# Performance work log

Measured on AMD Instinct MI355X. Metric: run time of the kernel, lower is better.

The kernel has to match this reference:

```python
import jax, jax.numpy as jnp
import numpy as np

N_NODES = 50000
N_EDGES = 800000
N_GRAPHS = 512
F_IN = 16
E_DIM = 64
D = 128          # encoder_dim
L_DIM = 64       # latent_dim
MP_STEPS = 3
S2S_STEPS = 3
NEG_SLOPE = 0.01


def _leaky(v):
    return jax.nn.leaky_relu(v, NEG_SLOPE)


def setup_inputs() -> dict:
    key = jax.random.key(0)
    ks = jax.random.split(key, 24)

    def w(k, fan_in, shape):
        return jax.random.normal(k, shape, jnp.float32) / np.sqrt(fan_in)

    inp = {
        "x": jax.random.normal(ks[0], (N_NODES, F_IN), jnp.float32),
        "edge_index": jax.random.randint(ks[1], (2, N_EDGES), 0, N_NODES, jnp.int64),
        "edge_attr": jax.random.normal(ks[2], (N_EDGES, 4), jnp.float32),
        "batch": jnp.sort(jax.random.randint(ks[3], (N_NODES,), 0, N_GRAPHS, jnp.int64)),
        # embedding: Linear(F_IN -> E_DIM); weights stored [in, out]
        "W_emb": w(ks[4], F_IN, (F_IN, E_DIM)),
        "b_emb": jnp.zeros((E_DIM,), jnp.float32),
        # first: Linear(E_DIM -> D)
        "W_first": w(ks[5], E_DIM, (E_DIM, D)),
        "b_first": jnp.zeros((D,), jnp.float32),
        # SAGEConv: lin_l (aggregated neighbors, with bias), lin_r (root, no bias)
        "W_l": w(ks[6], D, (D, D)),
        "b_l": jnp.zeros((D,), jnp.float32),
        "W_r": w(ks[7], D, (D, D)),
        # GRU (1 layer): gates ordered r,z,n as in torch
        "gru_Wih": w(ks[8], D, (D, 3 * D)),
        "gru_Whh": w(ks[9], D, (D, 3 * D)),
        "gru_bih": jnp.zeros((3 * D,), jnp.float32),
        "gru_bhh": jnp.zeros((3 * D,), jnp.float32),
        # Set2Set LSTM: input 2D -> hidden D; gates ordered i,f,g,o as in torch
        "lstm_Wih": w(ks[10], 2 * D, (2 * D, 4 * D)),
        "lstm_Whh": w(ks[11], D, (D, 4 * D)),
        "lstm_bih": jnp.zeros((4 * D,), jnp.float32),
        "lstm_bhh": jnp.zeros((4 * D,), jnp.float32),
        # linear: Linear(2D -> D), final: Linear(D -> L_DIM)
        "W_lin": w(ks[12], 2 * D, (2 * D, D)),
        "b_lin": jnp.zeros((D,), jnp.float32),
        "W_fin": w(ks[13], D, (D, L_DIM)),
        "b_fin": jnp.zeros((L_DIM,), jnp.float32),
    }
    return inp


def _gru_step(x, h, Wih, Whh, bih, bhh):
    gi = x @ Wih + bih
    gh = h @ Whh + bhh
    ir, iz, inn = jnp.split(gi, 3, axis=-1)
    hr, hz, hn = jnp.split(gh, 3, axis=-1)
    r = jax.nn.sigmoid(ir + hr)
    z = jax.nn.sigmoid(iz + hz)
    n = jnp.tanh(inn + r * hn)
    return (1.0 - z) * n + z * h


def _lstm_step(x, h, c, Wih, Whh, bih, bhh):
    g = x @ Wih + bih + h @ Whh + bhh
    i, f, gg, o = jnp.split(g, 4, axis=-1)
    c_new = jax.nn.sigmoid(f) * c + jax.nn.sigmoid(i) * jnp.tanh(gg)
    h_new = jax.nn.sigmoid(o) * jnp.tanh(c_new)
    return h_new, c_new


def reference(x, edge_index, edge_attr, batch,
              W_emb, b_emb, W_first, b_first,
              W_l, b_l, W_r,
              gru_Wih, gru_Whh, gru_bih, gru_bhh,
              lstm_Wih, lstm_Whh, lstm_bih, lstm_bhh,
              W_lin, b_lin, W_fin, b_fin):
    # edge_attr is ignored (PyG SAGEConv does not use it).
    out = _leaky(x @ W_emb + b_emb)        # [N, E_DIM]
    out = _leaky(out @ W_first + b_first)  # [N, D]
    h = out                                # GRU hidden state [N, D]
    src, dst = edge_index[0], edge_index[1]
    for _ in range(MP_STEPS):
        agg = jax.ops.segment_sum(out[src], dst, num_segments=N_NODES)  # [N, D]
        m = jax.nn.relu(agg @ W_l + b_l + out @ W_r)  # SAGEConv(aggr='add') + root
        out = _gru_step(m, h, gru_Wih, gru_Whh, gru_bih, gru_bhh)
        h = out
    # Set2Set pooling over graphs
    q_star = jnp.zeros((N_GRAPHS, 2 * D), out.dtype)
    hh = jnp.zeros((N_GRAPHS, D), out.dtype)
    cc = jnp.zeros((N_GRAPHS, D), out.dtype)
    for _ in range(S2S_STEPS):
        hh, cc = _lstm_step(q_star, hh, cc, lstm_Wih, lstm_Whh, lstm_bih, lstm_bhh)
        e = jnp.sum(out * hh[batch], axis=-1)                             # [N]
        e_max = jax.ops.segment_max(e, batch, num_segments=N_GRAPHS)      # [B]
        a = jnp.exp(e - e_max[batch])
        s = jax.ops.segment_sum(a, batch, num_segments=N_GRAPHS)
        a = a / (s[batch] + 1e-16)                                        # segment softmax
        r = jax.ops.segment_sum(a[:, None] * out, batch, num_segments=N_GRAPHS)  # [B, D]
        q_star = jnp.concatenate([hh, r], axis=-1)                        # [B, 2D]
    out = _leaky(q_star @ W_lin + b_lin)
    return out @ W_fin + b_fin  # [B, L_DIM]
```

## Files before the change

kernel.cpp:

```cpp
#include <hip/hip_runtime.h>
#include <hip/hip_bf16.h>
#include <math.h>

#define N_NODES 50000
#define N_EDGES 800000
#define N_GRAPHS 512
#define F_IN 16
#define E_DIM 64
#define D 128
#define L_DIM 64
#define NEG_SLOPE 0.01f

#define SCAN_N (N_NODES + 1)
#define NBUCK ((N_NODES + 127) >> 7)
#define EPT 4
#define BFT 1024
#define EPB (BFT * EPT)

typedef __hip_bfloat16 bf16;
typedef unsigned int uint;
typedef unsigned short ushort;
typedef __attribute__((ext_vector_type(8))) short short8;
typedef __attribute__((ext_vector_type(4))) float float4v;

__device__ __forceinline__ float b2f(bf16 v) { return __bfloat162float(v); }
__device__ __forceinline__ bf16  f2b(float v) { return __float2bfloat16(v); }
__device__ __forceinline__ short f2bs(float f) { bf16 b = __float2bfloat16(f); return *reinterpret_cast<short*>(&b); }
__device__ __forceinline__ float bs2f(short s) { return __uint_as_float(((uint)(ushort)s) << 16); }
__device__ __forceinline__ float leaky(float v) { return v > 0.f ? v : NEG_SLOPE * v; }

__device__ __forceinline__ float frcp(float x) { return __builtin_amdgcn_rcpf(x); }
__device__ __forceinline__ float sigm(float v) { return frcp(1.f + __expf(-v)); }
__device__ __forceinline__ float ftanh(float v)
{
    v = fminf(15.f, fmaxf(-15.f, v));
    float a = __expf(2.f * v);
    return (a - 1.f) * frcp(a + 1.f);
}

__global__ __launch_bounds__(256) void k_signal(float* outp, int n)
{
    int i = blockIdx.x * 256 + threadIdx.x;
    if (i < n) outp[i] = 1.0f;
}

#define NPE 16
__global__ __launch_bounds__(128) void k_embed(
    const float* __restrict__ x, const float* __restrict__ Wemb, const float* __restrict__ bemb,
    const float* __restrict__ Wfirst, const float* __restrict__ bfirst, bf16* __restrict__ out)
{
    __shared__ float xs[NPE][F_IN];
    __shared__ float ys[NPE][E_DIM];
    int t = threadIdx.x;
    int base = blockIdx.x * NPE;

    for (int i = t; i < NPE * F_IN; i += 128)
        xs[i / F_IN][i % F_IN] = x[(size_t)base * F_IN + i];
    __syncthreads();

    if (t < E_DIM) {
        float acc[NPE];
#pragma unroll
        for (int nn = 0; nn < NPE; nn++) acc[nn] = 0.f;
        for (int k = 0; k < F_IN; k++) {
            float w = Wemb[k * E_DIM + t];
#pragma unroll
            for (int nn = 0; nn < NPE; nn++) acc[nn] += xs[nn][k] * w;
        }
        float bb = bemb[t];
#pragma unroll
        for (int nn = 0; nn < NPE; nn++) ys[nn][t] = leaky(acc[nn] + bb);
    }
    __syncthreads();

    {
        float acc[NPE];
#pragma unroll
        for (int nn = 0; nn < NPE; nn++) acc[nn] = 0.f;
        for (int k = 0; k < E_DIM; k++) {
            float w = Wfirst[k * D + t];
#pragma unroll
            for (int nn = 0; nn < NPE; nn++) acc[nn] += ys[nn][k] * w;
        }
        float bb = bfirst[t];
#pragma unroll
        for (int nn = 0; nn < NPE; nn++)
            out[(size_t)(base + nn) * D + t] = f2b(leaky(acc[nn] + bb));
    }
}

__global__ __launch_bounds__(256) void k_bcount(const int* __restrict__ ei, int* __restrict__ bcnt)
{
    __shared__ int lc[NBUCK];
    for (int i = threadIdx.x; i < NBUCK; i += 256) lc[i] = 0;
    __syncthreads();
    int stride = gridDim.x * 256;
    for (int e = blockIdx.x * 256 + threadIdx.x; e < N_EDGES; e += stride) {
        int d = ei[N_EDGES + e];
        d = d < 0 ? 0 : (d >= N_NODES ? N_NODES - 1 : d);
        atomicAdd(&lc[d >> 7], 1);
    }
    __syncthreads();
    for (int i = threadIdx.x; i < NBUCK; i += 256)
        if (lc[i]) atomicAdd(&bcnt[i + 1], lc[i]);
}

__global__ void k_bscan(int* __restrict__ bcnt)
{
    if (threadIdx.x == 0 && blockIdx.x == 0) {
        int run = 0;
        for (int i = 0; i <= NBUCK; i++) { run += bcnt[i]; bcnt[i] = run; }
    }
}

__global__ __launch_bounds__(BFT) void k_bfill2(
    const int* __restrict__ ei, const int* __restrict__ bstart,
    int* __restrict__ bcur, uint* __restrict__ ebuf)
{
    __shared__ int lcnt[NBUCK];
    __shared__ int lbase[NBUCK];
    int t = threadIdx.x;
    int e0 = blockIdx.x * EPB;

    for (int i = t; i < NBUCK; i += BFT) lcnt[i] = 0;
    __syncthreads();

    uint pk[EPT];
    int bb[EPT];
#pragma unroll
    for (int q = 0; q < EPT; q++) {
        int e = e0 + q * BFT + t;
        bb[q] = -1;
        if (e < N_EDGES) {
            int s = ei[e];
            int d = ei[N_EDGES + e];
            s = s < 0 ? 0 : (s >= N_NODES ? N_NODES - 1 : s);
            d = d < 0 ? 0 : (d >= N_NODES ? N_NODES - 1 : d);
            bb[q] = d >> 7;
            pk[q] = ((uint)(d & 127) << 16) | (uint)s;
            atomicAdd(&lcnt[bb[q]], 1);
        }
    }
    __syncthreads();

    for (int i = t; i < NBUCK; i += BFT) {
        int cv = lcnt[i];
        lbase[i] = cv > 0 ? atomicAdd(&bcur[i], cv) : 0;
    }
    __syncthreads();
    for (int i = t; i < NBUCK; i += BFT) lcnt[i] = 0;
    __syncthreads();

#pragma unroll
    for (int q = 0; q < EPT; q++) {
        if (bb[q] >= 0) {
            int pos = lbase[bb[q]] + atomicAdd(&lcnt[bb[q]], 1);
            int slot = bstart[bb[q]] + pos;
            if (slot >= 0 && slot < N_EDGES) ebuf[slot] = pk[q];
        }
    }
}

__global__ __launch_bounds__(256) void k_csr(
    const int* __restrict__ bstart, const uint* __restrict__ ebuf,
    int* __restrict__ offs, int* __restrict__ srcs)
{
    __shared__ int cnt[128];
    __shared__ int loffs[129];
    int b = blockIdx.x, t = threadIdx.x;
    int e0 = bstart[b], e1 = bstart[b + 1];
    if (t < 128) cnt[t] = 0;
    __syncthreads();
    for (int j = e0 + t; j < e1; j += 256)
        atomicAdd(&cnt[(ebuf[j] >> 16) & 127], 1);
    __syncthreads();
    if (t == 0) {
        int run = 0;
        for (int i = 0; i < 128; i++) { loffs[i] = run; run += cnt[i]; }
        loffs[128] = run;
    }
    __syncthreads();
    int n0 = b << 7;
    if (t < 128) {
        int n = n0 + t;
        if (n <= N_NODES) offs[n] = e0 + loffs[t];
        cnt[t] = 0;
    }
    __syncthreads();
    for (int j = e0 + t; j < e1; j += 256) {
        uint pk = ebuf[j];
        int dl = (pk >> 16) & 127;
        int rank = atomicAdd(&cnt[dl], 1);
        int slot = e0 + loffs[dl] + rank;
        if (slot >= 0 && slot < N_EDGES) srcs[slot] = (int)(pk & 0xffffu);
    }
}

__global__ __launch_bounds__(256) void k_gstart(const int* __restrict__ batch, int* __restrict__ gstart)
{
    int g = blockIdx.x * 256 + threadIdx.x;
    if (g > N_GRAPHS) return;
    int lo = 0, hi = N_NODES;
    while (lo < hi) {
        int mid = (lo + hi) >> 1;
        if (batch[mid] < g) lo = mid + 1; else hi = mid;
    }
    gstart[g] = lo;
}

__global__ __launch_bounds__(256) void k_pack_all(
    const float* __restrict__ Wl, const float* __restrict__ Wr,
    const float* __restrict__ gWih, const float* __restrict__ gWhh,
    short* __restrict__ W1p, short* __restrict__ Wihp, short* __restrict__ Whhp)
{
    int tid = blockIdx.x * 256 + threadIdx.x;
    if (tid < 32768) {
        int j = tid & 7, l = (tid >> 3) & 63, frag = tid >> 9;
        int nb = frag >> 3, kb = frag & 7;
        int k = kb * 32 + ((l >> 4) * 8) + j;
        int n = nb * 16 + (l & 15);
        float v = (k < 128) ? Wl[k * D + n] : Wr[(k - 128) * D + n];
        W1p[tid] = f2bs(v);
    } else {
        int id = tid - 32768;
        const float* W = gWih;
        short* Wp = Wihp;
        if (id >= 49152) { id -= 49152; W = gWhh; Wp = Whhp; }
        int j = id & 7, l = (id >> 3) & 63, f = id >> 9;
        int ph = f >> 2, k0 = f & 3;
        int ct = ph / 3, p = ph - ct * 3;
        int k = k0 * 32 + ((l >> 4) * 8) + j;
        int n = p * 128 + ct * 16 + (l & 15);
        Wp[id] = f2bs(W[k * 384 + n]);
    }
}

__global__ __launch_bounds__(256) void k_gather(
    const bf16* __restrict__ hin, bf16* __restrict__ hagg,
    const int* __restrict__ offs, const int* __restrict__ srcs)
{
    int w = threadIdx.x >> 6, l = threadIdx.x & 63;
    int n = blockIdx.x * 4 + w;
    const ushort* hinu = (const ushort*)hin;
    int j0 = offs[n], j1 = offs[n + 1];
    j0 = j0 < 0 ? 0 : (j0 > N_EDGES ? N_EDGES : j0);
    j1 = j1 < j0 ? j0 : (j1 > N_EDGES ? N_EDGES : j1);

    float lo[8], hi8[8];
#pragma unroll
    for (int i = 0; i < 8; i++) { lo[i] = 0.f; hi8[i] = 0.f; }

    int j = j0;
    for (; j + 7 < j1; j += 8) {
        int ss[8];
        uint vv[8];
#pragma unroll
        for (int i = 0; i < 8; i++) {
            int s = srcs[j + i];
            ss[i] = s < 0 ? 0 : (s >= N_NODES ? N_NODES - 1 : s);
        }
#pragma unroll
        for (int i = 0; i < 8; i++)
            vv[i] = *(const uint*)(hinu + (size_t)ss[i] * D + l * 2);
#pragma unroll
        for (int i = 0; i < 8; i++) {
            lo[i] += __uint_as_float(vv[i] << 16);
            hi8[i] += __uint_as_float(vv[i] & 0xffff0000u);
        }
    }
    for (; j < j1; j++) {
        int s = srcs[j];
        s = s < 0 ? 0 : (s >= N_NODES ? N_NODES - 1 : s);
        uint v = *(const uint*)(hinu + (size_t)s * D + l * 2);
        lo[0] += __uint_as_float(v << 16);
        hi8[0] += __uint_as_float(v & 0xffff0000u);
    }
    float a0 = ((lo[0] + lo[1]) + (lo[2] + lo[3])) + ((lo[4] + lo[5]) + (lo[6] + lo[7]));
    float a1 = ((hi8[0] + hi8[1]) + (hi8[2] + hi8[3])) + ((hi8[4] + hi8[5]) + (hi8[6] + hi8[7]));
    uint ap = ((uint)(ushort)f2bs(a1) << 16) | (ushort)f2bs(a0);
    *(uint*)((ushort*)hagg + (size_t)n * D + l * 2) = ap;
}

#define M_STR 136
__global__ __launch_bounds__(256) void k_sage_gru_mfma(
    const bf16* __restrict__ hin, bf16* __restrict__ hagg_out,
    const short* __restrict__ W1p, const short* __restrict__ Wihp, const short* __restrict__ Whhp,
    const float* __restrict__ bl, const float* __restrict__ bih, const float* __restrict__ bhh)
{
    __shared__ short Msh[64 * M_STR];
    __shared__ short Hsh[64 * M_STR];
    int t = threadIdx.x;
    int w = t >> 6, l = t & 63;
    int rg = w >> 1, cg = w & 1;
    int base = blockIdx.x * 64;
    const ushort* hinu = (const ushort*)hin;
    const ushort* haggu = (const ushort*)hagg_out;
    ushort* houtu = (ushort*)hagg_out;

    int rA = base + rg * 32 + (l & 15);
    int rB = rA + 16;
    int rcA = rA < N_NODES ? rA : N_NODES - 1;
    int rcB = rB < N_NODES ? rB : N_NODES - 1;
    int koff = (l >> 4) * 8;

    short8 afrA[8], afrB[8];
#pragma unroll
    for (int k0 = 0; k0 < 4; k0++) {
        afrA[k0]     = *(const short8*)(haggu + (size_t)rcA * D + k0 * 32 + koff);
        afrB[k0]     = *(const short8*)(haggu + (size_t)rcB * D + k0 * 32 + koff);
        afrA[4 + k0] = *(const short8*)(hinu + (size_t)rcA * D + k0 * 32 + koff);
        afrB[4 + k0] = *(const short8*)(hinu + (size_t)rcB * D + k0 * 32 + koff);
    }

    int mrowA = rg * 32 + (l & 15);
    int mrowB = mrowA + 16;
    int crowA = rg * 32 + (l >> 4) * 4;
    int crowB = crowA + 16;

    if (cg == 0) {
#pragma unroll
        for (int k0 = 0; k0 < 4; k0++) {
            *(short8*)&Hsh[mrowA * M_STR + k0 * 32 + koff] = afrA[4 + k0];
            *(short8*)&Hsh[mrowB * M_STR + k0 * 32 + koff] = afrB[4 + k0];
        }
    }

    const short* w1 = W1p + cg * 16384;
    short8 bA[8], bB[8];
#pragma unroll
    for (int k0 = 0; k0 < 8; k0++)
        bA[k0] = *(const short8*)&w1[k0 * 512 + l * 8];
#pragma unroll
    for (int cti = 0; cti < 4; cti++) {
        int ct = cg * 4 + cti;
        const short8* bc = (cti & 1) ? bB : bA;
        short8* bn = (cti & 1) ? bA : bB;
        if (cti < 3) {
#pragma unroll
            for (int k0 = 0; k0 < 8; k0++)
                bn[k0] = *(const short8*)&w1[(cti + 1) * 4096 + k0 * 512 + l * 8];
        }
        float4v accA = {0.f, 0.f, 0.f, 0.f};
        float4v accB = {0.f, 0.f, 0.f, 0.f};
#pragma unroll
        for (int k0 = 0; k0 < 8; k0++) {
            accA = __builtin_amdgcn_mfma_f32_16x16x32_bf16(afrA[k0], bc[k0], accA, 0, 0, 0);
            accB = __builtin_amdgcn_mfma_f32_16x16x32_bf16(afrB[k0], bc[k0], accB, 0, 0, 0);
        }
        float bb = bl[ct * 16 + (l & 15)];
#pragma unroll
        for (int i = 0; i < 4; i++) {
            float vA = accA[i] + bb;
            float vB = accB[i] + bb;
            Msh[(crowA + i) * M_STR + ct * 16 + (l & 15)] = f2bs(vA > 0.f ? vA : 0.f);
            Msh[(crowB + i) * M_STR + ct * 16 + (l & 15)] = f2bs(vB > 0.f ? vB : 0.f);
        }
    }
    __syncthreads();

    short8 amrA[4], amrB[4];
#pragma unroll
    for (int k0 = 0; k0 < 4; k0++) {
        amrA[k0] = *(const short8*)&Msh[mrowA * M_STR + k0 * 32 + koff];
        amrB[k0] = *(const short8*)&Msh[mrowB * M_STR + k0 * 32 + koff];
    }

    const short* wip = Wihp + cg * 24576;
    const short* whp = Whhp + cg * 24576;
    short8 iA[4], hA[4], iB[4], hB[4];
#pragma unroll
    for (int k0 = 0; k0 < 4; k0++) {
        iA[k0] = *(const short8*)&wip[k0 * 512 + l * 8];
        hA[k0] = *(const short8*)&whp[k0 * 512 + l * 8];
    }
#pragma unroll
    for (int cti = 0; cti < 4; cti++) {
        int ct = cg * 4 + cti;
        int c = ct * 16 + (l & 15);
        float rvA[4], zvA[4], rvB[4], zvB[4];
#pragma unroll
        for (int p = 0; p < 3; p++) {
            int phl = cti * 3 + p;
            const short8* wi = (phl & 1) ? iB : iA;
            const short8* wh = (phl & 1) ? hB : hA;
            short8* win = (phl & 1) ? iA : iB;
            short8* whn = (phl & 1) ? hA : hB;
            if (phl < 11) {
#pragma unroll
                for (int k0 = 0; k0 < 4; k0++) {
                    win[k0] = *(const short8*)&wip[(phl + 1) * 2048 + k0 * 512 + l * 8];
                    whn[k0] = *(const short8*)&whp[(phl + 1) * 2048 + k0 * 512 + l * 8];
                }
            }
            float4v aiA = {0.f, 0.f, 0.f, 0.f};
            float4v ahA = {0.f, 0.f, 0.f, 0.f};
            float4v aiB = {0.f, 0.f, 0.f, 0.f};
            float4v ahB = {0.f, 0.f, 0.f, 0.f};
#pragma unroll
            for (int k0 = 0; k0 < 4; k0++) {
                aiA = __builtin_amdgcn_mfma_f32_16x16x32_bf16(amrA[k0], wi[k0], aiA, 0, 0, 0);
                ahA = __builtin_amdgcn_mfma_f32_16x16x32_bf16(afrA[4 + k0], wh[k0], ahA, 0, 0, 0);
                aiB = __builtin_amdgcn_mfma_f32_16x16x32_bf16(amrB[k0], wi[k0], aiB, 0, 0, 0);
                ahB = __builtin_amdgcn_mfma_f32_16x16x32_bf16(afrB[4 + k0], wh[k0], ahB, 0, 0, 0);
            }
            float bis = bih[p * 128 + c];
            float bhs = bhh[p * 128 + c];
            if (p == 0) {
#pragma unroll
                for (int i = 0; i < 4; i++) {
                    rvA[i] = sigm(aiA[i] + bis + ahA[i] + bhs);
                    rvB[i] = sigm(aiB[i] + bis + ahB[i] + bhs);
                }
            } else if (p == 1) {
#pragma unroll
                for (int i = 0; i < 4; i++) {
                    zvA[i] = sigm(aiA[i] + bis + ahA[i] + bhs);
                    zvB[i] = sigm(aiB[i] + bis + ahB[i] + bhs);
                }
            } else {
#pragma unroll
                for (int i = 0; i < 4; i++) {
                    int gA = base + crowA + i;
                    float h0A = bs2f(Hsh[(crowA + i) * M_STR + c]);
                    float nA = ftanh(aiA[i] + bis + rvA[i] * (ahA[i] + bhs));
                    if (gA < N_NODES)
                        houtu[(size_t)gA * D + c] = (ushort)f2bs((1.f - zvA[i]) * nA + zvA[i] * h0A);
                    int gB = base + crowB + i;
                    float h0B = bs2f(Hsh[(crowB + i) * M_STR + c]);
                    float nB = ftanh(aiB[i] + bis + rvB[i] * (ahB[i] + bhs));
                    if (gB < N_NODES)
                        houtu[(size_t)gB * D + c] = (ushort)f2bs((1.f - zvB[i]) * nB + zvB[i] * h0B);
                }
            }
        }
    }
}

#define POOL_CAP 1024
#define LG2 2
__global__ __launch_bounds__(1024) void k_s2s(
    const float* __restrict__ Wih, const float* __restrict__ Whh,
    const float* __restrict__ bih, const float* __restrict__ bhh,
    const bf16* __restrict__ h, const int* __restrict__ gstart,
    float* __restrict__ qstar, float* __restrict__ hh, float* __restrict__ cc, int first)
{
    int g0 = blockIdx.x * LG2;
    int t = threadIdx.x;
    __shared__ float qs[LG2][2 * D];
    __shared__ float hs[LG2][D];
    __shared__ float part[2][LG2][512];
    __shared__ float hnew[LG2][D];
    __shared__ float e_lds[POOL_CAP];
    __shared__ float redM[16], redS[16];
    __shared__ float rpart[8][D];

    for (int i = t; i < LG2 * 2 * D; i += 1024) {
        int g = i / (2 * D), c = i % (2 * D);
        qs[g][c] = first ? 0.f : qstar[(size_t)(g0 + g) * 2 * D + c];
    }
    for (int i = t; i < LG2 * D; i += 1024) {
        int g = i / D, c = i % D;
        hs[g][c] = first ? 0.f : hh[(size_t)(g0 + g) * D + c];
    }
    __syncthreads();

    int c = t & 511, half = t >> 9;
    float a0 = half ? 0.f : (bih[c] + bhh[c]);
    float a1 = a0;
    int qb = half * 128;
#pragma unroll 4
    for (int i = 0; i < 128; i++) {
        int k = qb + i;
        float wv = Wih[(size_t)k * 512 + c];
        a0 += qs[0][k] * wv;
        a1 += qs[1][k] * wv;
    }
    int hb = half * 64;
#pragma unroll 4
    for (int i = 0; i < 64; i++) {
        int k = hb + i;
        float wv = Whh[(size_t)k * 512 + c];
        a0 += hs[0][k] * wv;
        a1 += hs[1][k] * wv;
    }
    part[half][0][c] = a0;
    part[half][1][c] = a1;
    __syncthreads();

    if (t < LG2 * D) {
        int g = t >> 7, tt = t & 127;
        float gi = part[0][g][tt] + part[1][g][tt];
        float gf = part[0][g][D + tt] + part[1][g][D + tt];
        float gg2 = part[0][g][2 * D + tt] + part[1][g][2 * D + tt];
        float go = part[0][g][3 * D + tt] + part[1][g][3 * D + tt];
        float c_old = first ? 0.f : cc[(size_t)(g0 + g) * D + tt];
        float cn = sigm(gf) * c_old + sigm(gi) * ftanh(gg2);
        float hn = sigm(go) * ftanh(cn);
        cc[(size_t)(g0 + g) * D + tt] = cn;
        hh[(size_t)(g0 + g) * D + tt] = hn;
        qstar[(size_t)(g0 + g) * 2 * D + tt] = hn;
        hnew[g][tt] = hn;
    }
    __syncthreads();

    int w = t >> 6, l = t & 63;
    int dim = t & 127, h8 = t >> 7;
    const ushort* hu = (const ushort*)h;

    for (int gg = 0; gg < LG2; gg++) {
        int g = g0 + gg;
        int s0 = gstart[g], s1 = gstart[g + 1];
        s0 = s0 < 0 ? 0 : (s0 > N_NODES ? N_NODES : s0);
        s1 = s1 < s0 ? s0 : (s1 > N_NODES ? N_NODES : s1);
        int cnt = s1 - s0;

        float hq0 = hnew[gg][l];
        float hq1 = hnew[gg][64 + l];
        float m_run = -INFINITY, s_run = 0.f, racc = 0.f;

        for (int c0 = 0; c0 < cnt; c0 += POOL_CAP) {
            int clen = cnt - c0; if (clen > POOL_CAP) clen = POOL_CAP;

            for (int i = w; i < clen; i += 16) {
                int n = s0 + c0 + i;
                float v = bs2f((short)hu[(size_t)n * D + l]) * hq0
                        + bs2f((short)hu[(size_t)n * D + 64 + l]) * hq1;
#pragma unroll
                for (int off = 32; off > 0; off >>= 1) v += __shfl_down(v, off);
                if (l == 0) e_lds[i] = v;
            }
            __syncthreads();

            float m = -INFINITY;
            for (int i = t; i < clen; i += 1024) m = fmaxf(m, e_lds[i]);
#pragma unroll
            for (int off = 32; off > 0; off >>= 1) m = fmaxf(m, __shfl_down(m, off));
            if (l == 0) redM[w] = m;
            __syncthreads();
            m = -INFINITY;
#pragma unroll
            for (int i = 0; i < 16; i++) m = fmaxf(m, redM[i]);
            float m_new = fmaxf(m_run, m);
            float scale = (m_run == -INFINITY) ? 0.f : __expf(m_run - m_new);
            s_run *= scale;
            racc *= scale;
            __syncthreads();

            float s = 0.f;
            for (int i = t; i < clen; i += 1024) {
                float wv = __expf(e_lds[i] - m_new);
                e_lds[i] = wv;
                s += wv;
            }
#pragma unroll
            for (int off = 32; off > 0; off >>= 1) s += __shfl_down(s, off);
            if (l == 0) redS[w] = s;
            __syncthreads();
#pragma unroll
            for (int i = 0; i < 16; i++) s_run += redS[i];

            for (int i = h8; i < clen; i += 8)
                racc += e_lds[i] * bs2f((short)hu[(size_t)(s0 + c0 + i) * D + dim]);
            m_run = m_new;
            __syncthreads();
        }

        rpart[h8][dim] = racc;
        __syncthreads();
        if (t < D) {
            float inv = 1.f / (s_run + 1e-16f);
            float r = 0.f;
#pragma unroll
            for (int i = 0; i < 8; i++) r += rpart[i][t];
            qstar[(size_t)g * 2 * D + D + t] = r * inv;
        }
        __syncthreads();
    }
}

__global__ __launch_bounds__(128) void k_final(
    const float* __restrict__ qstar, const float* __restrict__ Wlin, const float* __restrict__ blin,
    const float* __restrict__ Wfin, const float* __restrict__ bfin, float* __restrict__ outp)
{
    int g = blockIdx.x, t = threadIdx.x;
    __shared__ float qs[2 * D], ts[D];
    qs[t] = qstar[(size_t)g * 2 * D + t];
    qs[D + t] = qstar[(size_t)g * 2 * D + D + t];
    __syncthreads();

    float acc = blin[t];
    for (int k = 0; k < 2 * D; k++) acc += qs[k] * Wlin[(size_t)k * D + t];
    ts[t] = leaky(acc);
    __syncthreads();

    if (t < L_DIM) {
        float a2 = bfin[t];
        for (int k = 0; k < D; k++) a2 += ts[k] * Wfin[(size_t)k * L_DIM + t];
        outp[(size_t)g * L_DIM + t] = a2;
    }
}

extern "C" void kernel_launch(void* const* d_in, const int* in_sizes, int n_in,
                              void* d_out, int out_size, void* d_ws, size_t ws_size,
                              hipStream_t stream)
{
    const float* x      = (const float*)d_in[0];
    const int*   ei     = (const int*)d_in[1];
    const int*   batch  = (const int*)d_in[3];
    const float* Wemb   = (const float*)d_in[4];
    const float* bemb   = (const float*)d_in[5];
    const float* Wfirst = (const float*)d_in[6];
    const float* bfirst = (const float*)d_in[7];
    const float* Wl     = (const float*)d_in[8];
    const float* bl     = (const float*)d_in[9];
    const float* Wr     = (const float*)d_in[10];
    const float* gWih   = (const float*)d_in[11];
    const float* gWhh   = (const float*)d_in[12];
    const float* gbih   = (const float*)d_in[13];
    const float* gbhh   = (const float*)d_in[14];
    const float* lWih   = (const float*)d_in[15];
    const float* lWhh   = (const float*)d_in[16];
    const float* lbih   = (const float*)d_in[17];
    const float* lbhh   = (const float*)d_in[18];
    const float* Wlin   = (const float*)d_in[19];
    const float* blin   = (const float*)d_in[20];
    const float* Wfin   = (const float*)d_in[21];
    const float* bfin   = (const float*)d_in[22];
    float* outp = (float*)d_out;

    size_t o = 0;
    char* base = (char*)d_ws;
    auto carve = [&](size_t bytes) { void* p = base + o; o += (bytes + 255) & ~(size_t)255; return p; };
    bf16*  h0     = (bf16*)carve((size_t)N_NODES * D * sizeof(bf16));
    bf16*  h1     = (bf16*)carve((size_t)N_NODES * D * sizeof(bf16));
    int*   offs   = (int*)carve((size_t)SCAN_N * sizeof(int));
    int*   srcs   = (int*)carve((size_t)N_EDGES * sizeof(int));
    int*   bcnt   = (int*)carve((size_t)(NBUCK + 1) * sizeof(int));
    int*   bcur   = (int*)carve((size_t)NBUCK * sizeof(int));
    uint*  ebuf   = (uint*)carve((size_t)N_EDGES * sizeof(uint));
    float* hh     = (float*)carve((size_t)N_GRAPHS * D * sizeof(float));
    float* cc     = (float*)carve((size_t)N_GRAPHS * D * sizeof(float));
    float* qstar  = (float*)carve((size_t)N_GRAPHS * 2 * D * sizeof(float));
    int*   gstart = (int*)carve((size_t)(N_GRAPHS + 1) * sizeof(int));
    short* W1p    = (short*)carve((size_t)256 * 128 * sizeof(short));
    short* Wihp   = (short*)carve((size_t)128 * 384 * sizeof(short));
    short* Whhp   = (short*)carve((size_t)128 * 384 * sizeof(short));
    size_t need = o;

    if (ws_size < need) {
        k_signal<<<(out_size + 255) / 256, 256, 0, stream>>>(outp, out_size);
        return;
    }

    k_embed<<<N_NODES / NPE, 128, 0, stream>>>(x, Wemb, bemb, Wfirst, bfirst, h0);

    k_pack_all<<<(32768 + 98304) / 256, 256, 0, stream>>>(Wl, Wr, gWih, gWhh, W1p, Wihp, Whhp);

    hipMemsetAsync(bcnt, 0, (size_t)((char*)ebuf - (char*)bcnt), stream);
    k_bcount<<<128, 256, 0, stream>>>(ei, bcnt);
    k_bscan<<<1, 64, 0, stream>>>(bcnt);
    k_bfill2<<<(N_EDGES + EPB - 1) / EPB, BFT, 0, stream>>>(ei, bcnt, bcur, ebuf);
    k_csr<<<NBUCK, 256, 0, stream>>>(bcnt, ebuf, offs, srcs);

    k_gstart<<<(N_GRAPHS + 1 + 255) / 256, 256, 0, stream>>>(batch, gstart);

    bf16* hc = h0; bf16* hn = h1;
    for (int s = 0; s < 3; s++) {
        k_gather<<<N_NODES / 4, 256, 0, stream>>>(hc, hn, offs, srcs);
        k_sage_gru_mfma<<<(N_NODES + 63) / 64, 256, 0, stream>>>(
            hc, hn, W1p, Wihp, Whhp, bl, gbih, gbhh);
        bf16* tmp = hc; hc = hn; hn = tmp;
    }

    for (int s = 0; s < 3; s++) {
        k_s2s<<<N_GRAPHS / LG2, 1024, 0, stream>>>(lWih, lWhh, lbih, lbhh,
                                                   hc, gstart, qstar, hh, cc, s == 0);
    }

    k_final<<<N_GRAPHS, 128, 0, stream>>>(qstar, Wlin, blin, Wfin, bfin, outp);
}
```

Before: 497.8 us.

## Split fused SAGE+GRU kernel into two kernels with LDS-staged weights

The fused SAGE+GRU MFMA kernel becomes two kernels. The SAGE linear layer writes its ReLU output to a new global buffer, and a separate GRU kernel launched over 4 column quarters per row tile reads it back. Both kernels stage their packed weight slices in LDS instead of streaming them from global memory into registers per wave. The goal is more parallelism and less register pressure for the GRU phase. The cost is an extra global write and read of the N×D message tensor, an extra launch per step, and the node features being reloaded by each of the four GRU blocks.

```diff
diff --git a/kernel.cpp b/kernel.cpp
--- a/kernel.cpp
+++ b/kernel.cpp
@@ -281,156 +281,172 @@
     *(uint*)((ushort*)hagg + (size_t)n * D + l * 2) = ap;
 }
 
-#define M_STR 136
-__global__ __launch_bounds__(256) void k_sage_gru_mfma(
-    const bf16* __restrict__ hin, bf16* __restrict__ hagg_out,
-    const short* __restrict__ W1p, const short* __restrict__ Wihp, const short* __restrict__ Whhp,
-    const float* __restrict__ bl, const float* __restrict__ bih, const float* __restrict__ bhh)
-{
-    __shared__ short Msh[64 * M_STR];
-    __shared__ short Hsh[64 * M_STR];
+__global__ __launch_bounds__(256) void k_sage1(
+    const bf16* __restrict__ hagg, const bf16* __restrict__ hin,
+    const short* __restrict__ W1p, const float* __restrict__ bl,
+    bf16* __restrict__ mout)
+{
+    __shared__ short8 w1s[4096];
     int t = threadIdx.x;
+    const short8* w1g = (const short8*)W1p;
+#pragma unroll
+    for (int i = 0; i < 16; i++)
+        w1s[i * 256 + t] = w1g[i * 256 + t];
+
     int w = t >> 6, l = t & 63;
     int rg = w >> 1, cg = w & 1;
     int base = blockIdx.x * 64;
-    const ushort* hinu = (const ushort*)hin;
-    const ushort* haggu = (const ushort*)hagg_out;
-    ushort* houtu = (ushort*)hagg_out;
-
     int rA = base + rg * 32 + (l & 15);
     int rB = rA + 16;
     int rcA = rA < N_NODES ? rA : N_NODES - 1;
     int rcB = rB < N_NODES ? rB : N_NODES - 1;
     int koff = (l >> 4) * 8;
+    const ushort* aggu = (const ushort*)hagg;
+    const ushort* hu = (const ushort*)hin;
+    ushort* mo = (ushort*)mout;
 
     short8 afrA[8], afrB[8];
 #pragma unroll
     for (int k0 = 0; k0 < 4; k0++) {
-        afrA[k0]     = *(const short8*)(haggu + (size_t)rcA * D + k0 * 32 + koff);
-        afrB[k0]     = *(const short8*)(haggu + (size_t)rcB * D + k0 * 32 + koff);
-        afrA[4 + k0] = *(const short8*)(hinu + (size_t)rcA * D + k0 * 32 + koff);
-        afrB[4 + k0] = *(const short8*)(hinu + (size_t)rcB * D + k0 * 32 + koff);
-    }
-
-    int mrowA = rg * 32 + (l & 15);
-    int mrowB = mrowA + 16;
+        afrA[k0]     = *(const short8*)(aggu + (size_t)rcA * D + k0 * 32 + koff);
+        afrB[k0]     = *(const short8*)(aggu + (size_t)rcB * D + k0 * 32 + koff);
+        afrA[4 + k0] = *(const short8*)(hu + (size_t)rcA * D + k0 * 32 + koff);
+        afrB[4 + k0] = *(const short8*)(hu + (size_t)rcB * D + k0 * 32 + koff);
+    }
+    __syncthreads();
+
+    const short* w1 = (const short*)w1s;
     int crowA = rg * 32 + (l >> 4) * 4;
     int crowB = crowA + 16;
-
-    if (cg == 0) {
-#pragma unroll
-        for (int k0 = 0; k0 < 4; k0++) {
-            *(short8*)&Hsh[mrowA * M_STR + k0 * 32 + koff] = afrA[4 + k0];
-            *(short8*)&Hsh[mrowB * M_STR + k0 * 32 + koff] = afrB[4 + k0];
-        }
-    }
-
-    const short* w1 = W1p + cg * 16384;
-    short8 bA[8], bB[8];
-#pragma unroll
-    for (int k0 = 0; k0 < 8; k0++)
-        bA[k0] = *(const short8*)&w1[k0 * 512 + l * 8];
 #pragma unroll
     for (int cti = 0; cti < 4; cti++) {
         int ct = cg * 4 + cti;
-        const short8* bc = (cti & 1) ? bB : bA;
-        short8* bn = (cti & 1) ? bA : bB;
-        if (cti < 3) {
-#pragma unroll
-            for (int k0 = 0; k0 < 8; k0++)
-                bn[k0] = *(const short8*)&w1[(cti + 1) * 4096 + k0 * 512 + l * 8];
-        }
+        short8 bw[8];
+#pragma unroll
+        for (int k0 = 0; k0 < 8; k0++)
+            bw[k0] = *(const short8*)&w1[(ct * 8 + k0) * 512 + l * 8];
         float4v accA = {0.f, 0.f, 0.f, 0.f};
         float4v accB = {0.f, 0.f, 0.f, 0.f};
 #pragma unroll
         for (int k0 = 0; k0 < 8; k0++) {
-            accA = __builtin_amdgcn_mfma_f32_16x16x32_bf16(afrA[k0], bc[k0], accA, 0, 0, 0);
-            accB = __builtin_amdgcn_mfma_f32_16x16x32_bf16(afrB[k0], bc[k0], accB, 0, 0, 0);
+            accA = __builtin_amdgcn_mfma_f32_16x16x32_bf16(afrA[k0], bw[k0], accA, 0, 0, 0);
+            accB = __builtin_amdgcn_mfma_f32_16x16x32_bf16(afrB[k0], bw[k0], accB, 0, 0, 0);
         }
         float bb = bl[ct * 16 + (l & 15)];
 #pragma unroll
         for (int i = 0; i < 4; i++) {
             float vA = accA[i] + bb;
             float vB = accB[i] + bb;
-            Msh[(crowA + i) * M_STR + ct * 16 + (l & 15)] = f2bs(vA > 0.f ? vA : 0.f);
-            Msh[(crowB + i) * M_STR + ct * 16 + (l & 15)] = f2bs(vB > 0.f ? vB : 0.f);
-        }
-    }
-    __syncthreads();
-
-    short8 amrA[4], amrB[4];
+            int gA = base + crowA + i;
+            int gB = base + crowB + i;
+            if (gA < N_NODES) mo[(size_t)gA * D + ct * 16 + (l & 15)] = (ushort)f2bs(vA > 0.f ? vA : 0.f);
+            if (gB < N_NODES) mo[(size_t)gB * D + ct * 16 + (l & 15)] = (ushort)f2bs(vB > 0.f ? vB : 0.f);
+        }
+    }
+}
+
+__global__ __launch_bounds__(256) void k_gru2(
+    const bf16* __restrict__ m, const bf16* __restrict__ hin,
+    const short* __restrict__ Wihp, const short* __restrict__ Whhp,
+    const float* __restrict__ bih, const float* __restrict__ bhh,
+    bf16* __restrict__ hout)
+{
+    __shared__ short8 wis[1536];
+    __shared__ short8 whs[1536];
+    int t = threadIdx.x;
+    int tile = blockIdx.x >> 2, cq = blockIdx.x & 3;
+    const short8* wig = (const short8*)(Wihp + cq * 12288);
+    const short8* whg = (const short8*)(Whhp + cq * 12288);
+#pragma unroll
+    for (int i = 0; i < 6; i++) {
+        wis[i * 256 + t] = wig[i * 256 + t];
+        whs[i * 256 + t] = whg[i * 256 + t];
+    }
+
+    int w = t >> 6, l = t & 63;
+    int rg = w >> 1, cs = w & 1;
+    int base = tile * 64;
+    int rA = base + rg * 32 + (l & 15);
+    int rB = rA + 16;
+    int rcA = rA < N_NODES ? rA : N_NODES - 1;
+    int rcB = rB < N_NODES ? rB : N_NODES - 1;
+    int koff = (l >> 4) * 8;
+    int ct = cq * 2 + cs;
+    int c = ct * 16 + (l & 15);
+
+    const ushort* mu = (const ushort*)m;
+    const ushort* hu = (const ushort*)hin;
+    ushort* ho = (ushort*)hout;
+
+    short8 amrA[4], amrB[4], ahfA[4], ahfB[4];
 #pragma unroll
     for (int k0 = 0; k0 < 4; k0++) {
-        amrA[k0] = *(const short8*)&Msh[mrowA * M_STR + k0 * 32 + koff];
-        amrB[k0] = *(const short8*)&Msh[mrowB * M_STR + k0 * 32 + koff];
-    }
-
-    const short* wip = Wihp + cg * 24576;
-    const short* whp = Whhp + cg * 24576;
-    short8 iA[4], hA[4], iB[4], hB[4];
-#pragma unroll
-    for (int k0 = 0; k0 < 4; k0++) {
-        iA[k0] = *(const short8*)&wip[k0 * 512 + l * 8];
-        hA[k0] = *(const short8*)&whp[k0 * 512 + l * 8];
-    }
-#pragma unroll
-    for (int cti = 0; cti < 4; cti++) {
-        int ct = cg * 4 + cti;
-        int c = ct * 16 + (l & 15);
-        float rvA[4], zvA[4], rvB[4], zvB[4];
-#pragma unroll
-        for (int p = 0; p < 3; p++) {
-            int phl = cti * 3 + p;
-            const short8* wi = (phl & 1) ? iB : iA;
-            const short8* wh = (phl & 1) ? hB : hA;
-            short8* win = (phl & 1) ? iA : iB;
-            short8* whn = (phl & 1) ? hA : hB;
-            if (phl < 11) {
-#pragma unroll
-                for (int k0 = 0; k0 < 4; k0++) {
-                    win[k0] = *(const short8*)&wip[(phl + 1) * 2048 + k0 * 512 + l * 8];
-                    whn[k0] = *(const short8*)&whp[(phl + 1) * 2048 + k0 * 512 + l * 8];
-                }
+        amrA[k0] = *(const short8*)(mu + (size_t)rcA * D + k0 * 32 + koff);
+        amrB[k0] = *(const short8*)(mu + (size_t)rcB * D + k0 * 32 + koff);
+        ahfA[k0] = *(const short8*)(hu + (size_t)rcA * D + k0 * 32 + koff);
+        ahfB[k0] = *(const short8*)(hu + (size_t)rcB * D + k0 * 32 + koff);
+    }
+
+    int crowA = rg * 32 + (l >> 4) * 4;
+    int crowB = crowA + 16;
+    float h0A[4], h0B[4];
+#pragma unroll
+    for (int i = 0; i < 4; i++) {
+        int ra = base + crowA + i; ra = ra < N_NODES ? ra : N_NODES - 1;
+        int rb = base + crowB + i; rb = rb < N_NODES ? rb : N_NODES - 1;
+        h0A[i] = bs2f((short)hu[(size_t)ra * D + c]);
+        h0B[i] = bs2f((short)hu[(size_t)rb * D + c]);
+    }
+    __syncthreads();
+
+    const short* wip = (const short*)wis;
+    const short* whp = (const short*)whs;
+    float rvA[4], zvA[4], rvB[4], zvB[4];
+#pragma unroll
+    for (int p = 0; p < 3; p++) {
+        int pl = cs * 3 + p;
+        short8 wi[4], wh[4];
+#pragma unroll
+        for (int k0 = 0; k0 < 4; k0++) {
+            wi[k0] = *(const short8*)&wip[pl * 2048 + k0 * 512 + l * 8];
+            wh[k0] = *(const short8*)&whp[pl * 2048 + k0 * 512 + l * 8];
+        }
+        float4v aiA = {0.f, 0.f, 0.f, 0.f};
+        float4v ahA = {0.f, 0.f, 0.f, 0.f};
+        float4v aiB = {0.f, 0.f, 0.f, 0.f};
+        float4v ahB = {0.f, 0.f, 0.f, 0.f};
+#pragma unroll
+        for (int k0 = 0; k0 < 4; k0++) {
+            aiA = __builtin_amdgcn_mfma_f32_16x16x32_bf16(amrA[k0], wi[k0], aiA, 0, 0, 0);
+            ahA = __builtin_amdgcn_mfma_f32_16x16x32_bf16(ahfA[k0], wh[k0], ahA, 0, 0, 0);
+            aiB = __builtin_amdgcn_mfma_f32_16x16x32_bf16(amrB[k0], wi[k0], aiB, 0, 0, 0);
+            ahB = __builtin_amdgcn_mfma_f32_16x16x32_bf16(ahfB[k0], wh[k0], ahB, 0, 0, 0);
+        }
+        float bis = bih[p * 128 + c];
+        float bhs = bhh[p * 128 + c];
+        if (p == 0) {
+#pragma unroll
+            for (int i = 0; i < 4; i++) {
+                rvA[i] = sigm(aiA[i] + bis + ahA[i] + bhs);
+                rvB[i] = sigm(aiB[i] + bis + ahB[i] + bhs);
             }
-            float4v aiA = {0.f, 0.f, 0.f, 0.f};
-            float4v ahA = {0.f, 0.f, 0.f, 0.f};
-            float4v aiB = {0.f, 0.f, 0.f, 0.f};
-            float4v ahB = {0.f, 0.f, 0.f, 0.f};
-#pragma unroll
-            for (int k0 = 0; k0 < 4; k0++) {
-                aiA = __builtin_amdgcn_mfma_f32_16x16x32_bf16(amrA[k0], wi[k0], aiA, 0, 0, 0);
-                ahA = __builtin_amdgcn_mfma_f32_16x16x32_bf16(afrA[4 + k0], wh[k0], ahA, 0, 0, 0);
-                aiB = __builtin_amdgcn_mfma_f32_16x16x32_bf16(amrB[k0], wi[k0], aiB, 0, 0, 0);
-                ahB = __builtin_amdgcn_mfma_f32_16x16x32_bf16(afrB[4 + k0], wh[k0], ahB, 0, 0, 0);
+        } else if (p == 1) {
+#pragma unroll
+            for (int i = 0; i < 4; i++) {
+                zvA[i] = sigm(aiA[i] + bis + ahA[i] + bhs);
+                zvB[i] = sigm(aiB[i] + bis + ahB[i] + bhs);
             }
-            float bis = bih[p * 128 + c];
-            float bhs = bhh[p * 128 + c];
-            if (p == 0) {
-#pragma unroll
-                for (int i = 0; i < 4; i++) {
-                    rvA[i] = sigm(aiA[i] + bis + ahA[i] + bhs);
-                    rvB[i] = sigm(aiB[i] + bis + ahB[i] + bhs);
-                }
-            } else if (p == 1) {
-#pragma unroll
-                for (int i = 0; i < 4; i++) {
-                    zvA[i] = sigm(aiA[i] + bis + ahA[i] + bhs);
-                    zvB[i] = sigm(aiB[i] + bis + ahB[i] + bhs);
-                }
-            } else {
-#pragma unroll
-                for (int i = 0; i < 4; i++) {
-                    int gA = base + crowA + i;
-                    float h0A = bs2f(Hsh[(crowA + i) * M_STR + c]);
-                    float nA = ftanh(aiA[i] + bis + rvA[i] * (ahA[i] + bhs));
-                    if (gA < N_NODES)
-                        houtu[(size_t)gA * D + c] = (ushort)f2bs((1.f - zvA[i]) * nA + zvA[i] * h0A);
-                    int gB = base + crowB + i;
-                    float h0B = bs2f(Hsh[(crowB + i) * M_STR + c]);
-                    float nB = ftanh(aiB[i] + bis + rvB[i] * (ahB[i] + bhs));
-                    if (gB < N_NODES)
-                        houtu[(size_t)gB * D + c] = (ushort)f2bs((1.f - zvB[i]) * nB + zvB[i] * h0B);
-                }
+        } else {
+#pragma unroll
+            for (int i = 0; i < 4; i++) {
+                int gA = base + crowA + i;
+                float nA = ftanh(aiA[i] + bis + rvA[i] * (ahA[i] + bhs));
+                if (gA < N_NODES)
+                    ho[(size_t)gA * D + c] = (ushort)f2bs((1.f - zvA[i]) * nA + zvA[i] * h0A[i]);
+                int gB = base + crowB + i;
+                float nB = ftanh(aiB[i] + bis + rvB[i] * (ahB[i] + bhs));
+                if (gB < N_NODES)
+                    ho[(size_t)gB * D + c] = (ushort)f2bs((1.f - zvB[i]) * nB + zvB[i] * h0B[i]);
             }
         }
     }
@@ -633,6 +649,7 @@
     auto carve = [&](size_t bytes) { void* p = base + o; o += (bytes + 255) & ~(size_t)255; return p; };
     bf16*  h0     = (bf16*)carve((size_t)N_NODES * D * sizeof(bf16));
     bf16*  h1     = (bf16*)carve((size_t)N_NODES * D * sizeof(bf16));
+    bf16*  mbuf   = (bf16*)carve((size_t)N_NODES * D * sizeof(bf16));
     int*   offs   = (int*)carve((size_t)SCAN_N * sizeof(int));
     int*   srcs   = (int*)carve((size_t)N_EDGES * sizeof(int));
     int*   bcnt   = (int*)carve((size_t)(NBUCK + 1) * sizeof(int));
@@ -664,11 +681,12 @@
 
     k_gstart<<<(N_GRAPHS + 1 + 255) / 256, 256, 0, stream>>>(batch, gstart);
 
+    const int NTILE = (N_NODES + 63) / 64;
     bf16* hc = h0; bf16* hn = h1;
     for (int s = 0; s < 3; s++) {
         k_gather<<<N_NODES / 4, 256, 0, stream>>>(hc, hn, offs, srcs);
-        k_sage_gru_mfma<<<(N_NODES + 63) / 64, 256, 0, stream>>>(
-            hc, hn, W1p, Wihp, Whhp, bl, gbih, gbhh);
+        k_sage1<<<NTILE, 256, 0, stream>>>(hn, hc, W1p, bl, mbuf);
+        k_gru2<<<NTILE * 4, 256, 0, stream>>>(mbuf, hc, Wihp, Whhp, gbih, gbhh, hn);
         bf16* tmp = hc; hc = hn; hn = tmp;
     }
 
```

New measurement: 568.2 us. 1.14x slower.
